# Kernel optimization log

Measured on AMD Instinct MI355X. Metric: run time of the kernel, lower is better.

## Reference

```python
import jax, jax.numpy as jnp
import numpy as np

N_HEADS = 8
D_HEAD = 64
SCALE = D_HEAD ** -0.5


def setup_inputs() -> dict:
    key = jax.random.key(0)
    k1, k2, k3 = jax.random.split(key, 3)
    B, H, W, C = 16, 32, 32, 512
    ft = jax.random.normal(k1, (B, H, W, C), dtype=jnp.float32)
    # Dense layers: to_qkv -> n_heads*n_dim_heads*3 = 1536 units, to_out -> n_channels
    w_qkv = jax.random.normal(k2, (C, N_HEADS * D_HEAD * 3), dtype=jnp.float32) * (C ** -0.5)
    b_qkv = jnp.zeros((N_HEADS * D_HEAD * 3,), dtype=jnp.float32)
    w_out = jax.random.normal(k3, (N_HEADS * D_HEAD, C), dtype=jnp.float32) * ((N_HEADS * D_HEAD) ** -0.5)
    b_out = jnp.zeros((C,), dtype=jnp.float32)
    return {"ft": ft, "w_qkv": w_qkv, "b_qkv": b_qkv, "w_out": w_out, "b_out": b_out}


def reference(ft, w_qkv, b_qkv, w_out, b_out):
    B, H, W, C = ft.shape
    N = H * W
    x = ft.reshape(B, N, C)                       # b (h w) c
    qkv = x @ w_qkv + b_qkv                       # b n (heads * 3*d_head)
    qkv = qkv.reshape(B, N, N_HEADS, 3 * D_HEAD)  # 'b x (h d) -> b x h d'
    q, k, v = jnp.split(qkv, 3, axis=-1)          # each: b n heads d_head
    attn = jnp.einsum('bxhd,byhd->bxyh', q, k) * SCALE
    attn = jax.nn.softmax(attn, axis=2)           # softmax over key axis y
    res = jnp.einsum('bxyh,byhd->bxhd', attn, v)  # b x h d
    res = res.reshape(B, N, N_HEADS * D_HEAD)     # 'b x h d -> b x (h d)'
    res = res @ w_out + b_out
    res = res + x                                 # residual with pre-qkv flattened input
    return res.reshape(B, H, W, C)
```

## Files before the change

kernel.cpp:

```cpp
#include <hip/hip_runtime.h>
#include <hip/hip_bf16.h>

using u16 = unsigned short;
using u32 = unsigned int;
typedef __attribute__((ext_vector_type(8))) short short8;
typedef __attribute__((ext_vector_type(4))) float f32x4;

#define MFMA16(A, B, C) __builtin_amdgcn_mfma_f32_16x16x32_bf16((A), (B), (C), 0, 0, 0)

__device__ __forceinline__ u16 f2bf(float f) {
  union { float f; u32 i; } v; v.f = f;
  u32 x = v.i;
  return (u16)((x + 0x7fffu + ((x >> 16) & 1u)) >> 16);
}
__device__ __forceinline__ u32 pkbf(float a, float b) {
  union { __hip_bfloat162 h; u32 u; } v;
  v.h = __float22bfloat162_rn(make_float2(a, b));
  return v.u;
}
__device__ __forceinline__ u32 cvtpk(float a, float b) {
  u32 r;
  asm("v_cvt_pk_bf16_f32 %0, %1, %2" : "=v"(r) : "v"(a), "v"(b));
  return r;
}
__device__ __forceinline__ void gl16(const u16* g, u16* l) {
  __builtin_amdgcn_global_load_lds(
      (const __attribute__((address_space(1))) u32*)g,
      (__attribute__((address_space(3))) u32*)l, 16, 0, 0);
}

__global__ __launch_bounds__(256) void conv_x(const float* __restrict__ X,
                                              u16* __restrict__ Xbf) {
  const int i = (blockIdx.x * 256 + threadIdx.x) * 8;
  float4 a = *(const float4*)(X + i);
  float4 b = *(const float4*)(X + i + 4);
  uint4 o;
  o.x = pkbf(a.x, a.y); o.y = pkbf(a.z, a.w);
  o.z = pkbf(b.x, b.y); o.w = pkbf(b.z, b.w);
  *(uint4*)(Xbf + i) = o;
}

__global__ __launch_bounds__(256) void transpose_w(
    const float* __restrict__ Wq, const float* __restrict__ Wo,
    u16* __restrict__ Wqt, u16* __restrict__ Wot) {
  const int z = blockIdx.z;
  if (z == 1 && blockIdx.x >= 16) return;
  const float* src = z ? Wo : Wq;
  u16* dst = z ? Wot : Wqt;
  const int ncols = z ? 512 : 1536;
  __shared__ float tile[32][33];
  const int t = threadIdx.x;
  const int kt = blockIdx.y * 32, nt = blockIdx.x * 32;
  const int r = t >> 3, c4 = (t & 7) * 4;
  float4 v = *(const float4*)(src + (size_t)(kt + r) * ncols + nt + c4);
  tile[r][c4 + 0] = v.x; tile[r][c4 + 1] = v.y;
  tile[r][c4 + 2] = v.z; tile[r][c4 + 3] = v.w;
  __syncthreads();
  uint2 p = make_uint2(pkbf(tile[c4 + 0][r], tile[c4 + 1][r]),
                       pkbf(tile[c4 + 2][r], tile[c4 + 3][r]));
  *(uint2*)(dst + (size_t)(nt + r) * 512 + kt + c4) = p;
}

__global__ __launch_bounds__(512) void qkv_gemm(
    const u16* __restrict__ Xbf, const u16* __restrict__ Wt,
    const float* __restrict__ Bias,
    u16* __restrict__ Qp, u16* __restrict__ Kp, u16* __restrict__ Vt) {
  __shared__ u16 Xs[3][128][32];
  __shared__ u16 Ws[3][256][32];
  const int t = threadIdx.x;
  const int lid = blockIdx.y * 6 + blockIdx.x;
  const int sid = (lid & 7) * 96 + (lid >> 3);
  const int bm = (sid / 6) * 128, bn = (sid % 6) * 256;
  const int w = t >> 6, lane = t & 63, quad = lane >> 4, l16 = lane & 15;
  const int mtb = (w >> 2) * 64, ntb = (w & 3) * 64;
  const int rr = lane >> 2;
  const int gch = ((lane & 3) ^ ((lane >> 3) & 3)) * 8;
  const int sw = (quad ^ ((l16 >> 1) & 3)) * 8;

  const u16* xg0 = Xbf + (size_t)(bm + w * 16 + rr) * 512 + gch;
  const u16* wg0 = Wt + (size_t)(bn + w * 16 + rr) * 512 + gch;
  const u16* wg1 = wg0 + (size_t)128 * 512;

  f32x4 acc[4][4];
  const f32x4 z4 = {0.f, 0.f, 0.f, 0.f};
  #pragma unroll
  for (int mi = 0; mi < 4; mi++)
    #pragma unroll
    for (int ni = 0; ni < 4; ni++) acc[mi][ni] = z4;

  gl16(xg0, &Xs[0][w * 16][0]);
  gl16(wg0, &Ws[0][w * 16][0]); gl16(wg1, &Ws[0][w * 16][0] + 4096);
  gl16(xg0 + 32, &Xs[1][w * 16][0]);
  gl16(wg0 + 32, &Ws[1][w * 16][0]); gl16(wg1 + 32, &Ws[1][w * 16][0] + 4096);
  asm volatile("s_waitcnt vmcnt(3)" ::: "memory");
  __builtin_amdgcn_s_barrier();

  for (int k = 0; k < 16; ++k) {
    const int cur = k % 3;
    if (k < 14) {
      const int nx2 = (k + 2) % 3;
      const int kn = (k + 2) * 32;
      gl16(xg0 + kn, &Xs[nx2][w * 16][0]);
      gl16(wg0 + kn, &Ws[nx2][w * 16][0]);
      gl16(wg1 + kn, &Ws[nx2][w * 16][0] + 4096);
    }
    short8 af[4], bf4[4];
    #pragma unroll
    for (int mi = 0; mi < 4; mi++)
      af[mi] = *(const short8*)&Xs[cur][mtb + mi * 16 + l16][sw];
    #pragma unroll
    for (int ni = 0; ni < 4; ni++)
      bf4[ni] = *(const short8*)&Ws[cur][ntb + ni * 16 + l16][sw];
    #pragma unroll
    for (int mi = 0; mi < 4; mi++)
      #pragma unroll
      for (int ni = 0; ni < 4; ni++)
        acc[mi][ni] = MFMA16(af[mi], bf4[ni], acc[mi][ni]);
    if (k < 15) {
      if (k < 14) asm volatile("s_waitcnt vmcnt(3) lgkmcnt(0)" ::: "memory");
      else        asm volatile("s_waitcnt vmcnt(0) lgkmcnt(0)" ::: "memory");
      __builtin_amdgcn_s_barrier();
    }
  }

  #pragma unroll
  for (int ni = 0; ni < 4; ni++) {
    const int g = bn + ntb + ni * 16;
    const int h = g / 192, rm = g % 192;
    const int type = rm >> 6, dbase = rm & 63;
    const float bias = Bias[g + l16];
    const float qsc = (type == 0) ? 0.125f * 1.44269504088896340736f : 1.0f;
    #pragma unroll
    for (int mi = 0; mi < 4; mi++) {
      const int row0 = bm + mtb + mi * 16 + quad * 4;
      const int b = row0 >> 10, n0 = row0 & 1023;
      const size_t bh = (size_t)(b * 8 + h) * 65536;
      if (type == 2) {
        uint2 p = make_uint2(pkbf(acc[mi][ni][0] + bias, acc[mi][ni][1] + bias),
                             pkbf(acc[mi][ni][2] + bias, acc[mi][ni][3] + bias));
        *(uint2*)(Vt + bh + (size_t)(dbase + l16) * 1024 + n0) = p;
      } else {
        u16* dst = (type ? Kp : Qp) + bh;
        #pragma unroll
        for (int r = 0; r < 4; r++)
          dst[(size_t)(n0 + r) * 64 + dbase + l16] =
              f2bf((acc[mi][ni][r] + bias) * qsc);
      }
    }
  }
}

__global__ __launch_bounds__(512, 8) void attn_mfma(
    const u16* __restrict__ Qp, const u16* __restrict__ Kp,
    const u16* __restrict__ Vt, u16* __restrict__ ATT) {
  __shared__ u16 Ks[2][64][64];
  __shared__ u16 Vs[2][64][64];
  const int t = threadIdx.x, w = t >> 6, lane = t & 63;
  const int quad = lane >> 4, l16 = lane & 15;
  const int bx = blockIdx.x;
  const int c = bx & 7, g = bx >> 3;
  const int qt = g & 7, u = g >> 3;
  const int bh_id = u * 8 + c;
  const int b = bh_id >> 3, h = bh_id & 7;
  const size_t bh = (size_t)bh_id * 65536;
  const u16* Qb = Qp + bh;
  const u16* Kb = Kp + bh;
  const u16* Vb = Vt + bh;
  const int q0 = qt * 128 + w * 16;

  const u16* kg = Kb + (size_t)(t >> 3) * 64 + ((t & 7) ^ ((t >> 3) & 7)) * 8;
  const u16* vg = Vb + (size_t)(t >> 3) * 1024 + ((t & 7) ^ ((t >> 3) & 7)) * 8;
  u16* ks0 = &Ks[0][0][0] + w * 512;
  u16* ks1 = &Ks[1][0][0] + w * 512;
  u16* vs0 = &Vs[0][0][0] + w * 512;
  u16* vs1 = &Vs[1][0][0] + w * 512;

  const int m7 = l16 & 7;
  const char* ksb = (const char*)&Ks[0][0][0];
  const char* vsb = (const char*)&Vs[0][0][0];
  const int kb0 = l16 * 128 + (quad ^ m7) * 16;
  const int kb1 = kb0 ^ 64;
  int vo[2];
  #pragma unroll
  for (int ks = 0; ks < 2; ks++)
    vo[ks] = l16 * 128 + ((4 * ks + quad) ^ m7) * 16;

  short8 qf[2];
  #pragma unroll
  for (int ks = 0; ks < 2; ks++)
    qf[ks] = *(const short8*)(Qb + (size_t)(q0 + l16) * 64 + ks * 32 + quad * 8);

  float l_ = 0.f;
  f32x4 Of[4];
  const f32x4 z4 = {0.f, 0.f, 0.f, 0.f};
  #pragma unroll
  for (int ni = 0; ni < 4; ni++) Of[ni] = z4;

  gl16(kg, ks0);
  gl16(vg, vs0);
  __syncthreads();

  for (int kt = 0; kt < 16; ++kt) {
    const int cur = kt & 1;
    if (kt < 15) {
      gl16(kg + (kt + 1) * 4096, cur ? ks0 : ks1);
      gl16(vg + (kt + 1) * 64,   cur ? vs0 : vs1);
    }
    const int co = cur << 13;

    u32 e[4], o[4];
    #pragma unroll
    for (int nt = 0; nt < 4; nt++) {
      short8 k0f = *(const short8*)(ksb + co + kb0 + nt * 2048);
      short8 k1f = *(const short8*)(ksb + co + kb1 + nt * 2048);
      f32x4 s = z4;
      s = MFMA16(k0f, qf[0], s);
      s = MFMA16(k1f, qf[1], s);
      float p0 = __builtin_amdgcn_exp2f(s[0]);
      float p1 = __builtin_amdgcn_exp2f(s[1]);
      float p2 = __builtin_amdgcn_exp2f(s[2]);
      float p3 = __builtin_amdgcn_exp2f(s[3]);
      l_ += (p0 + p1) + (p2 + p3);
      const u32 lo = cvtpk(p0, p1), hi = cvtpk(p2, p3);
      if (nt & 1) { o[(nt >> 1) * 2] = lo; o[(nt >> 1) * 2 + 1] = hi; }
      else        { e[(nt >> 1) * 2] = lo; e[(nt >> 1) * 2 + 1] = hi; }
    }
    #pragma unroll
    for (int i = 0; i < 4; i++) {
      auto t01 = __builtin_amdgcn_permlane32_swap(e[i], o[i], false, false);
      auto xy  = __builtin_amdgcn_permlane16_swap(t01[0], t01[1], false, false);
      e[i] = xy[0]; o[i] = xy[1];
    }
    #pragma unroll
    for (int ks = 0; ks < 2; ks++) {
      union { short8 v; u32 u[4]; } pa;
      pa.u[0] = e[2 * ks]; pa.u[1] = e[2 * ks + 1];
      pa.u[2] = o[2 * ks]; pa.u[3] = o[2 * ks + 1];
      #pragma unroll
      for (int ni = 0; ni < 4; ni++) {
        short8 vf = *(const short8*)(vsb + co + vo[ks] + ni * 2048);
        Of[ni] = MFMA16(pa.v, vf, Of[ni]);
      }
    }
    __syncthreads();
  }
  l_ += __shfl_xor(l_, 16);
  l_ += __shfl_xor(l_, 32);
  float lv[4];
  #pragma unroll
  for (int r = 0; r < 4; r++) lv[r] = __shfl(l_, quad * 4 + r);
  #pragma unroll
  for (int r = 0; r < 4; r++) {
    const float inv = 1.0f / lv[r];
    const int row = b * 1024 + q0 + quad * 4 + r;
    #pragma unroll
    for (int ni = 0; ni < 4; ni++)
      ATT[(size_t)row * 512 + h * 64 + ni * 16 + l16] = f2bf(Of[ni][r] * inv);
  }
}

__global__ __launch_bounds__(256) void out_proj(
    const u16* __restrict__ A, const u16* __restrict__ Wt,
    const float* __restrict__ Bias, const float* __restrict__ FT,
    float* __restrict__ OUT) {
  __shared__ u16 As[3][128][32];
  __shared__ u16 Ws[3][128][32];
  const int t = threadIdx.x;
  const int lid = blockIdx.y * 4 + blockIdx.x;
  const int sid = (lid & 7) * 64 + (lid >> 3);
  const int bm = (sid / 4) * 128, bn = (sid % 4) * 128;
  const int w = t >> 6, lane = t & 63, quad = lane >> 4, l16 = lane & 15;
  const int mtb = (w >> 1) * 64, ntb = (w & 1) * 64;
  const int rr = lane >> 2;
  const int gch = ((lane & 3) ^ ((lane >> 3) & 3)) * 8;
  const int sw = (quad ^ ((l16 >> 1) & 3)) * 8;

  const u16* ag0 = A + (size_t)(bm + w * 16 + rr) * 512 + gch;
  const u16* ag1 = ag0 + (size_t)64 * 512;
  const u16* wg0 = Wt + (size_t)(bn + w * 16 + rr) * 512 + gch;
  const u16* wg1 = wg0 + (size_t)64 * 512;

  f32x4 acc[4][4];
  const f32x4 z4 = {0.f, 0.f, 0.f, 0.f};
  #pragma unroll
  for (int mi = 0; mi < 4; mi++)
    #pragma unroll
    for (int ni = 0; ni < 4; ni++) acc[mi][ni] = z4;

  gl16(ag0, &As[0][w * 16][0]); gl16(ag1, &As[0][w * 16][0] + 2048);
  gl16(wg0, &Ws[0][w * 16][0]); gl16(wg1, &Ws[0][w * 16][0] + 2048);
  gl16(ag0 + 32, &As[1][w * 16][0]); gl16(ag1 + 32, &As[1][w * 16][0] + 2048);
  gl16(wg0 + 32, &Ws[1][w * 16][0]); gl16(wg1 + 32, &Ws[1][w * 16][0] + 2048);
  asm volatile("s_waitcnt vmcnt(4)" ::: "memory");
  __builtin_amdgcn_s_barrier();

  for (int k = 0; k < 16; ++k) {
    const int cur = k % 3;
    if (k < 14) {
      const int nx2 = (k + 2) % 3;
      const int kn = (k + 2) * 32;
      gl16(ag0 + kn, &As[nx2][w * 16][0]);
      gl16(ag1 + kn, &As[nx2][w * 16][0] + 2048);
      gl16(wg0 + kn, &Ws[nx2][w * 16][0]);
      gl16(wg1 + kn, &Ws[nx2][w * 16][0] + 2048);
    }
    short8 af[4], bf4[4];
    #pragma unroll
    for (int mi = 0; mi < 4; mi++)
      af[mi] = *(const short8*)&As[cur][mtb + mi * 16 + l16][sw];
    #pragma unroll
    for (int ni = 0; ni < 4; ni++)
      bf4[ni] = *(const short8*)&Ws[cur][ntb + ni * 16 + l16][sw];
    #pragma unroll
    for (int mi = 0; mi < 4; mi++)
      #pragma unroll
      for (int ni = 0; ni < 4; ni++)
        acc[mi][ni] = MFMA16(af[mi], bf4[ni], acc[mi][ni]);
    if (k < 15) {
      if (k < 14) asm volatile("s_waitcnt vmcnt(4) lgkmcnt(0)" ::: "memory");
      else        asm volatile("s_waitcnt vmcnt(0) lgkmcnt(0)" ::: "memory");
      __builtin_amdgcn_s_barrier();
    }
  }

  #pragma unroll
  for (int ni = 0; ni < 4; ni++) {
    const int g = bn + ntb + ni * 16;
    const float bias = Bias[g + l16];
    #pragma unroll
    for (int mi = 0; mi < 4; mi++) {
      const int row0 = bm + mtb + mi * 16 + quad * 4;
      #pragma unroll
      for (int r = 0; r < 4; r++) {
        const size_t idx = (size_t)(row0 + r) * 512 + g + l16;
        OUT[idx] = acc[mi][ni][r] + bias + FT[idx];
      }
    }
  }
}

extern "C" void kernel_launch(void* const* d_in, const int* in_sizes, int n_in,
                              void* d_out, int out_size, void* d_ws, size_t ws_size,
                              hipStream_t stream) {
  const float* ft    = (const float*)d_in[0];
  const float* w_qkv = (const float*)d_in[1];
  const float* b_qkv = (const float*)d_in[2];
  const float* w_out = (const float*)d_in[3];
  const float* b_out = (const float*)d_in[4];
  float* out = (float*)d_out;

  char* p = (char*)d_ws;
  u16* Xbf    = (u16*)(p);
  u16* ATT    = Xbf;
  u16* Wqkv_t = (u16*)(p + 16777216);
  u16* Wout_t = (u16*)(p + 18350080);
  u16* Qp     = (u16*)(p + 18874368);
  u16* Kp     = (u16*)(p + 35651584);
  u16* Vt     = (u16*)(p + 52428800);

  conv_x     <<<4096, 256, 0, stream>>>(ft, Xbf);
  transpose_w<<<dim3(48, 16, 2), 256, 0, stream>>>(w_qkv, w_out, Wqkv_t, Wout_t);
  qkv_gemm   <<<dim3(6, 128), 512, 0, stream>>>(Xbf, Wqkv_t, b_qkv, Qp, Kp, Vt);
  attn_mfma  <<<dim3(1024), 512, 0, stream>>>(Qp, Kp, Vt, ATT);
  out_proj   <<<dim3(4, 128), 256, 0, stream>>>(ATT, Wout_t, b_out, ft, out);
}
```

Before: 195.8 us.

## Triple-buffer K tiles with fine-grained vmcnt waits and MFMA priority hints

The attention kernel now keeps three K buffers, prefetching K two tiles ahead and V one tile ahead. The full __syncthreads is replaced by an explicit s_waitcnt vmcnt(1) plus s_barrier, so only the oldest load must land before the barrier. s_setprio raises wave priority around the MFMA sections. This aims to hide global-load latency better, at the cost of 8KB more LDS per block and a fragile dependence on load issue order for the vmcnt counts.

```diff
diff --git a/kernel.cpp b/kernel.cpp
--- a/kernel.cpp
+++ b/kernel.cpp
@@ -153,7 +153,7 @@
 __global__ __launch_bounds__(512, 8) void attn_mfma(
     const u16* __restrict__ Qp, const u16* __restrict__ Kp,
     const u16* __restrict__ Vt, u16* __restrict__ ATT) {
-  __shared__ u16 Ks[2][64][64];
+  __shared__ u16 Ks[3][64][64];
   __shared__ u16 Vs[2][64][64];
   const int t = threadIdx.x, w = t >> 6, lane = t & 63;
   const int quad = lane >> 4, l16 = lane & 15;
@@ -170,10 +170,8 @@
 
   const u16* kg = Kb + (size_t)(t >> 3) * 64 + ((t & 7) ^ ((t >> 3) & 7)) * 8;
   const u16* vg = Vb + (size_t)(t >> 3) * 1024 + ((t & 7) ^ ((t >> 3) & 7)) * 8;
-  u16* ks0 = &Ks[0][0][0] + w * 512;
-  u16* ks1 = &Ks[1][0][0] + w * 512;
-  u16* vs0 = &Vs[0][0][0] + w * 512;
-  u16* vs1 = &Vs[1][0][0] + w * 512;
+  u16* ksW = &Ks[0][0][0] + w * 512;
+  u16* vsW = &Vs[0][0][0] + w * 512;
 
   const int m7 = l16 & 7;
   const char* ksb = (const char*)&Ks[0][0][0];
@@ -196,23 +194,25 @@
   #pragma unroll
   for (int ni = 0; ni < 4; ni++) Of[ni] = z4;
 
-  gl16(kg, ks0);
-  gl16(vg, vs0);
-  __syncthreads();
-
+  gl16(kg, ksW);
+  gl16(vg, vsW);
+  gl16(kg + 4096, ksW + 4096);
+  asm volatile("s_waitcnt vmcnt(1)" ::: "memory");
+  __builtin_amdgcn_s_barrier();
+
+  int c3 = 0, n3 = 2;
   for (int kt = 0; kt < 16; ++kt) {
-    const int cur = kt & 1;
-    if (kt < 15) {
-      gl16(kg + (kt + 1) * 4096, cur ? ks0 : ks1);
-      gl16(vg + (kt + 1) * 64,   cur ? vs0 : vs1);
-    }
-    const int co = cur << 13;
+    if (kt < 15) gl16(vg + (kt + 1) * 64, vsW + ((kt + 1) & 1) * 4096);
+    if (kt < 14) gl16(kg + (kt + 2) * 4096, ksW + n3 * 4096);
+    const int cok = c3 << 13;
+    const int cov = (kt & 1) << 13;
 
     u32 e[4], o[4];
+    __builtin_amdgcn_s_setprio(1);
     #pragma unroll
     for (int nt = 0; nt < 4; nt++) {
-      short8 k0f = *(const short8*)(ksb + co + kb0 + nt * 2048);
-      short8 k1f = *(const short8*)(ksb + co + kb1 + nt * 2048);
+      short8 k0f = *(const short8*)(ksb + cok + kb0 + nt * 2048);
+      short8 k1f = *(const short8*)(ksb + cok + kb1 + nt * 2048);
       f32x4 s = z4;
       s = MFMA16(k0f, qf[0], s);
       s = MFMA16(k1f, qf[1], s);
@@ -225,12 +225,14 @@
       if (nt & 1) { o[(nt >> 1) * 2] = lo; o[(nt >> 1) * 2 + 1] = hi; }
       else        { e[(nt >> 1) * 2] = lo; e[(nt >> 1) * 2 + 1] = hi; }
     }
+    __builtin_amdgcn_s_setprio(0);
     #pragma unroll
     for (int i = 0; i < 4; i++) {
       auto t01 = __builtin_amdgcn_permlane32_swap(e[i], o[i], false, false);
       auto xy  = __builtin_amdgcn_permlane16_swap(t01[0], t01[1], false, false);
       e[i] = xy[0]; o[i] = xy[1];
     }
+    __builtin_amdgcn_s_setprio(1);
     #pragma unroll
     for (int ks = 0; ks < 2; ks++) {
       union { short8 v; u32 u[4]; } pa;
@@ -238,11 +240,18 @@
       pa.u[2] = o[2 * ks]; pa.u[3] = o[2 * ks + 1];
       #pragma unroll
       for (int ni = 0; ni < 4; ni++) {
-        short8 vf = *(const short8*)(vsb + co + vo[ks] + ni * 2048);
+        short8 vf = *(const short8*)(vsb + cov + vo[ks] + ni * 2048);
         Of[ni] = MFMA16(pa.v, vf, Of[ni]);
       }
     }
-    __syncthreads();
+    __builtin_amdgcn_s_setprio(0);
+    if (kt < 15) {
+      if (kt < 14) asm volatile("s_waitcnt vmcnt(1) lgkmcnt(0)" ::: "memory");
+      else         asm volatile("s_waitcnt vmcnt(0) lgkmcnt(0)" ::: "memory");
+      __builtin_amdgcn_s_barrier();
+    }
+    c3 = (c3 == 2) ? 0 : c3 + 1;
+    n3 = (n3 == 2) ? 0 : n3 + 1;
   }
   l_ += __shfl_xor(l_, 16);
   l_ += __shfl_xor(l_, 32);
```

Measured after the change: 199.0 us. Within noise of the previous version (+1.6%).

## Compute softmax row sums via MFMA with ones and use 512-thread out_proj

Applied to the files above, without the earlier changes.

The attention kernel no longer accumulates the row sum of exponentials with scalar adds and cross-lane shuffles. It adds one extra MFMA per k-step that multiplies the bf16 probability tile by a ones vector, which yields row sums already in the output layout. The out_proj GEMM moves from 256 to 512 threads per 128x128 tile, with each wave owning a 32x64 sub-tile and issuing half the global loads, to raise wave-level parallelism. The row sum is now taken over bf16-rounded probabilities, which changes the numerics slightly, and the extra MFMA adds matrix work.

```diff
diff --git a/kernel.cpp b/kernel.cpp
--- a/kernel.cpp
+++ b/kernel.cpp
@@ -190,11 +190,15 @@
   for (int ks = 0; ks < 2; ks++)
     qf[ks] = *(const short8*)(Qb + (size_t)(q0 + l16) * 64 + ks * 32 + quad * 8);
 
-  float l_ = 0.f;
-  f32x4 Of[4];
+  const short8 vone = {(short)0x3F80, (short)0x3F80, (short)0x3F80,
+                       (short)0x3F80, (short)0x3F80, (short)0x3F80,
+                       (short)0x3F80, (short)0x3F80};
+
+  f32x4 Of[4], Ol;
   const f32x4 z4 = {0.f, 0.f, 0.f, 0.f};
   #pragma unroll
   for (int ni = 0; ni < 4; ni++) Of[ni] = z4;
+  Ol = z4;
 
   gl16(kg, ks0);
   gl16(vg, vs0);
@@ -220,7 +224,6 @@
       float p1 = __builtin_amdgcn_exp2f(s[1]);
       float p2 = __builtin_amdgcn_exp2f(s[2]);
       float p3 = __builtin_amdgcn_exp2f(s[3]);
-      l_ += (p0 + p1) + (p2 + p3);
       const u32 lo = cvtpk(p0, p1), hi = cvtpk(p2, p3);
       if (nt & 1) { o[(nt >> 1) * 2] = lo; o[(nt >> 1) * 2 + 1] = hi; }
       else        { e[(nt >> 1) * 2] = lo; e[(nt >> 1) * 2 + 1] = hi; }
@@ -241,17 +244,13 @@
         short8 vf = *(const short8*)(vsb + co + vo[ks] + ni * 2048);
         Of[ni] = MFMA16(pa.v, vf, Of[ni]);
       }
+      Ol = MFMA16(pa.v, vone, Ol);
     }
     __syncthreads();
   }
-  l_ += __shfl_xor(l_, 16);
-  l_ += __shfl_xor(l_, 32);
-  float lv[4];
-  #pragma unroll
-  for (int r = 0; r < 4; r++) lv[r] = __shfl(l_, quad * 4 + r);
   #pragma unroll
   for (int r = 0; r < 4; r++) {
-    const float inv = 1.0f / lv[r];
+    const float inv = 1.0f / Ol[r];
     const int row = b * 1024 + q0 + quad * 4 + r;
     #pragma unroll
     for (int ni = 0; ni < 4; ni++)
@@ -259,7 +258,7 @@
   }
 }
 
-__global__ __launch_bounds__(256) void out_proj(
+__global__ __launch_bounds__(512) void out_proj(
     const u16* __restrict__ A, const u16* __restrict__ Wt,
     const float* __restrict__ Bias, const float* __restrict__ FT,
     float* __restrict__ OUT) {
@@ -270,28 +269,24 @@
   const int sid = (lid & 7) * 64 + (lid >> 3);
   const int bm = (sid / 4) * 128, bn = (sid % 4) * 128;
   const int w = t >> 6, lane = t & 63, quad = lane >> 4, l16 = lane & 15;
-  const int mtb = (w >> 1) * 64, ntb = (w & 1) * 64;
+  const int mtb = (w >> 1) * 32, ntb = (w & 1) * 64;
   const int rr = lane >> 2;
   const int gch = ((lane & 3) ^ ((lane >> 3) & 3)) * 8;
   const int sw = (quad ^ ((l16 >> 1) & 3)) * 8;
 
-  const u16* ag0 = A + (size_t)(bm + w * 16 + rr) * 512 + gch;
-  const u16* ag1 = ag0 + (size_t)64 * 512;
-  const u16* wg0 = Wt + (size_t)(bn + w * 16 + rr) * 512 + gch;
-  const u16* wg1 = wg0 + (size_t)64 * 512;
-
-  f32x4 acc[4][4];
+  const u16* ag = A + (size_t)(bm + w * 16 + rr) * 512 + gch;
+  const u16* wg = Wt + (size_t)(bn + w * 16 + rr) * 512 + gch;
+
+  f32x4 acc[2][4];
   const f32x4 z4 = {0.f, 0.f, 0.f, 0.f};
   #pragma unroll
-  for (int mi = 0; mi < 4; mi++)
+  for (int mi = 0; mi < 2; mi++)
     #pragma unroll
     for (int ni = 0; ni < 4; ni++) acc[mi][ni] = z4;
 
-  gl16(ag0, &As[0][w * 16][0]); gl16(ag1, &As[0][w * 16][0] + 2048);
-  gl16(wg0, &Ws[0][w * 16][0]); gl16(wg1, &Ws[0][w * 16][0] + 2048);
-  gl16(ag0 + 32, &As[1][w * 16][0]); gl16(ag1 + 32, &As[1][w * 16][0] + 2048);
-  gl16(wg0 + 32, &Ws[1][w * 16][0]); gl16(wg1 + 32, &Ws[1][w * 16][0] + 2048);
-  asm volatile("s_waitcnt vmcnt(4)" ::: "memory");
+  gl16(ag, &As[0][w * 16][0]);      gl16(wg, &Ws[0][w * 16][0]);
+  gl16(ag + 32, &As[1][w * 16][0]); gl16(wg + 32, &Ws[1][w * 16][0]);
+  asm volatile("s_waitcnt vmcnt(2)" ::: "memory");
   __builtin_amdgcn_s_barrier();
 
   for (int k = 0; k < 16; ++k) {
@@ -299,25 +294,23 @@
     if (k < 14) {
       const int nx2 = (k + 2) % 3;
       const int kn = (k + 2) * 32;
-      gl16(ag0 + kn, &As[nx2][w * 16][0]);
-      gl16(ag1 + kn, &As[nx2][w * 16][0] + 2048);
-      gl16(wg0 + kn, &Ws[nx2][w * 16][0]);
-      gl16(wg1 + kn, &Ws[nx2][w * 16][0] + 2048);
-    }
-    short8 af[4], bf4[4];
-    #pragma unroll
-    for (int mi = 0; mi < 4; mi++)
+      gl16(ag + kn, &As[nx2][w * 16][0]);
+      gl16(wg + kn, &Ws[nx2][w * 16][0]);
+    }
+    short8 af[2], bf4[4];
+    #pragma unroll
+    for (int mi = 0; mi < 2; mi++)
       af[mi] = *(const short8*)&As[cur][mtb + mi * 16 + l16][sw];
     #pragma unroll
     for (int ni = 0; ni < 4; ni++)
       bf4[ni] = *(const short8*)&Ws[cur][ntb + ni * 16 + l16][sw];
     #pragma unroll
-    for (int mi = 0; mi < 4; mi++)
+    for (int mi = 0; mi < 2; mi++)
       #pragma unroll
       for (int ni = 0; ni < 4; ni++)
         acc[mi][ni] = MFMA16(af[mi], bf4[ni], acc[mi][ni]);
     if (k < 15) {
-      if (k < 14) asm volatile("s_waitcnt vmcnt(4) lgkmcnt(0)" ::: "memory");
+      if (k < 14) asm volatile("s_waitcnt vmcnt(2) lgkmcnt(0)" ::: "memory");
       else        asm volatile("s_waitcnt vmcnt(0) lgkmcnt(0)" ::: "memory");
       __builtin_amdgcn_s_barrier();
     }
@@ -328,7 +321,7 @@
     const int g = bn + ntb + ni * 16;
     const float bias = Bias[g + l16];
     #pragma unroll
-    for (int mi = 0; mi < 4; mi++) {
+    for (int mi = 0; mi < 2; mi++) {
       const int row0 = bm + mtb + mi * 16 + quad * 4;
       #pragma unroll
       for (int r = 0; r < 4; r++) {
@@ -362,5 +355,5 @@
   transpose_w<<<dim3(48, 16, 2), 256, 0, stream>>>(w_qkv, w_out, Wqkv_t, Wout_t);
   qkv_gemm   <<<dim3(6, 128), 512, 0, stream>>>(Xbf, Wqkv_t, b_qkv, Qp, Kp, Vt);
   attn_mfma  <<<dim3(1024), 512, 0, stream>>>(Qp, Kp, Vt, ATT);
-  out_proj   <<<dim3(4, 128), 256, 0, stream>>>(ATT, Wout_t, b_out, ft, out);
-}
+  out_proj   <<<dim3(4, 128), 512, 0, stream>>>(ATT, Wout_t, b_out, ft, out);
+}
```

Measured after the change: 189.6 us. -3.2%, faster.
